# Kernel optimization log

Hardware: AMD Instinct MI355X
Metric: run time of the kernel (lower is better)

The kernel has to match this reference:

```python
import jax, jax.numpy as jnp
import numpy as np

N_NODES = 100000
N_EDGES = 1600000
N_GRAPHS = 512
IN_CH = 128
HID = 128
OUT_CH = 1
FP_DIM = 2048


def prelu(x, a):
    return jnp.where(x > 0, x, a * x)


def setup_inputs() -> dict:
    key = jax.random.key(0)
    ks = jax.random.split(key, 16)

    def glorot(k, shape):
        lim = np.sqrt(6.0 / (shape[0] + shape[1]))
        return jax.random.uniform(k, shape, jnp.float32, -lim, lim)

    x = jax.random.normal(ks[0], (N_NODES, IN_CH), jnp.float32)
    fp = jax.random.normal(ks[1], (N_GRAPHS, FP_DIM), jnp.float32)
    edge_index = jax.random.randint(ks[2], (2, N_EDGES), 0, N_NODES, jnp.int64)
    batch = jnp.sort(jax.random.randint(ks[3], (N_NODES,), 0, N_GRAPHS, jnp.int64))

    params = {
        "W_pre": glorot(ks[4], (IN_CH, HID)),
        "b_pre": jnp.zeros((HID,), jnp.float32),
        "a_pre": jnp.full((HID,), 0.25, jnp.float32),
        "Wl1": glorot(ks[5], (HID, HID)),
        "bl1": jnp.zeros((HID,), jnp.float32),
        "Wr1": glorot(ks[6], (HID, HID)),
        "a1": jnp.full((HID,), 0.25, jnp.float32),
        "Wl2": glorot(ks[7], (HID, HID)),
        "bl2": jnp.zeros((HID,), jnp.float32),
        "Wr2": glorot(ks[8], (HID, HID)),
        "a2": jnp.full((HID,), 0.25, jnp.float32),
        "W_fp": glorot(ks[9], (FP_DIM, HID)),
        "b_fp": jnp.zeros((HID,), jnp.float32),
        "a_fp": jnp.full((HID,), 0.25, jnp.float32),
        "W_post": glorot(ks[10], (2 * HID, OUT_CH)),
        "b_post": jnp.zeros((OUT_CH,), jnp.float32),
    }
    return dict(x=x, fp=fp, edge_index=edge_index, batch=batch, **params)


def sage_conv(x, src, dst, Wl, bl, Wr):
    # aggr='sum': sum messages x[src] into dst, then lin_l(agg)+bias + lin_r(x)
    agg = jax.ops.segment_sum(x[src], dst, num_segments=N_NODES)  # [N, H]
    return agg @ Wl + bl + x @ Wr


def reference(x, fp, edge_index, batch,
              W_pre, b_pre, a_pre,
              Wl1, bl1, Wr1, a1,
              Wl2, bl2, Wr2, a2,
              W_fp, b_fp, a_fp,
              W_post, b_post):
    src, dst = edge_index[0], edge_index[1]
    # pre_mp (dropout is identity at eval)
    h = prelu(x @ W_pre + b_pre, a_pre)
    # message passing
    h = prelu(sage_conv(h, src, dst, Wl1, bl1, Wr1), a1)
    h = prelu(sage_conv(h, src, dst, Wl2, bl2, Wr2), a2)
    # global mean pool over graphs
    sums = jax.ops.segment_sum(h, batch, num_segments=N_GRAPHS)  # [G, H]
    counts = jax.ops.segment_sum(jnp.ones((h.shape[0],), h.dtype), batch,
                                 num_segments=N_GRAPHS)
    pooled = sums / jnp.maximum(counts, 1.0)[:, None]
    # fingerprint head
    fp_emb = prelu(fp @ W_fp + b_fp, a_fp)
    # post mp
    out = jnp.concatenate([pooled, fp_emb], axis=1) @ W_post + b_post
    return out
```

## Files before the change

kernel.cpp:

```cpp
#include <hip/hip_runtime.h>

#define NN 100000
#define NE 1600000
#define NG 512
#define HID 128
#define FPD 2048
#define BSHIFT 8
#define NBUK ((NN + 255) >> 8)
#define BCAP 5120
#define EPB 4096
#define EPT 16

typedef _Float16 f16;
typedef __attribute__((ext_vector_type(8))) _Float16 f16x8;
typedef __attribute__((ext_vector_type(2))) _Float16 f16x2;
typedef __attribute__((ext_vector_type(4))) float f32x4;


__global__ __launch_bounds__(256) void bucket_scatter(const int* __restrict__ src,
                                                      const int* __restrict__ dst,
                                                      int* __restrict__ bcnt,
                                                      uint* __restrict__ bbuf, int E) {
  __shared__ int hist[NBUK];
  __shared__ int gbase[NBUK];
  __shared__ int lbase[NBUK + 1];
  __shared__ int sc[2][512];
  __shared__ uint stage[EPB];
  int t = threadIdx.x;
  int e0 = blockIdx.x * EPB;
  for (int i = t; i < NBUK; i += 256) hist[i] = 0;
  __syncthreads();

  int myb[EPT], myoff[EPT];
  uint myp[EPT];
#pragma unroll
  for (int u = 0; u < EPT; ++u) {
    int e = e0 + u * 256 + t;
    myb[u] = -1;
    if (e < E) {
      int d = dst[e];
      int b = d >> BSHIFT;
      myp[u] = ((uint)(d & 255) << 24) | (uint)src[e];
      myb[u] = b;
      myoff[u] = atomicAdd(&hist[b], 1);
    }
  }
  __syncthreads();

  sc[0][t] = (t < NBUK) ? hist[t] : 0;
  sc[0][t + 256] = (t + 256 < NBUK) ? hist[t + 256] : 0;
  int pp = 0;
  for (int off = 1; off < 512; off <<= 1) {
    __syncthreads();
    int a0 = sc[pp][t] + ((t >= off) ? sc[pp][t - off] : 0);
    int a1 = sc[pp][t + 256] + ((t + 256 >= off) ? sc[pp][t + 256 - off] : 0);
    sc[1 - pp][t] = a0;
    sc[1 - pp][t + 256] = a1;
    pp = 1 - pp;
  }
  __syncthreads();
  if (t < NBUK) lbase[t] = (t == 0) ? 0 : sc[pp][t - 1];
  if (t + 256 < NBUK) lbase[t + 256] = sc[pp][t + 255];
  if (t == 0) lbase[NBUK] = sc[pp][NBUK - 1];
  for (int i = t; i < NBUK; i += 256)
    if (hist[i] > 0) gbase[i] = atomicAdd(&bcnt[i], hist[i]);
  __syncthreads();

#pragma unroll
  for (int u = 0; u < EPT; ++u)
    if (myb[u] >= 0) stage[lbase[myb[u]] + myoff[u]] = myp[u];
  __syncthreads();

  int total = lbase[NBUK];
  for (int j = t; j < total; j += 256) {
    int lo = 0, hi = NBUK - 1;
    while (lo < hi) {
      int mid = (lo + hi + 1) >> 1;
      if (lbase[mid] <= j) lo = mid; else hi = mid - 1;
    }
    bbuf[(size_t)lo * BCAP + gbase[lo] + (j - lbase[lo])] = stage[j];
  }
}

__global__ __launch_bounds__(512) void scan_bcnt(const int* __restrict__ bcnt,
                                                 int* __restrict__ bbase,
                                                 int* __restrict__ rowptr) {
  __shared__ int lds[512];
  int t = threadIdx.x;
  int v = (t < NBUK) ? bcnt[t] : 0;
  lds[t] = v;
  __syncthreads();
  for (int off = 1; off < 512; off <<= 1) {
    int add = (t >= off) ? lds[t - off] : 0;
    __syncthreads();
    lds[t] += add;
    __syncthreads();
  }
  if (t < NBUK) bbase[t] = lds[t] - v;
  if (t == 0) {
    bbase[NBUK] = lds[511];
    rowptr[NN] = lds[511];
  }
}

__global__ __launch_bounds__(256) void bucket_hist_scan(const int* __restrict__ bcnt,
                                                        const uint* __restrict__ bbuf,
                                                        const int* __restrict__ bbase,
                                                        int* __restrict__ rowptr) {
  __shared__ int h[256];
  __shared__ int lds[256];
  int b = blockIdx.x, t = threadIdx.x;
  h[t] = 0;
  __syncthreads();
  int n = bcnt[b];
  const uint* bb = bbuf + (size_t)b * BCAP;
  for (int e = t; e < n; e += 256) atomicAdd(&h[bb[e] >> 24], 1);
  __syncthreads();
  int v = h[t];
  lds[t] = v;
  __syncthreads();
  for (int off = 1; off < 256; off <<= 1) {
    int add = (t >= off) ? lds[t - off] : 0;
    __syncthreads();
    lds[t] += add;
    __syncthreads();
  }
  int node = (b << BSHIFT) + t;
  if (node < NN) rowptr[node] = bbase[b] + lds[t] - v;
}

__global__ __launch_bounds__(256) void bucket_place(const int* __restrict__ bcnt,
                                                    const uint* __restrict__ bbuf,
                                                    const int* __restrict__ rowptr,
                                                    int* __restrict__ cols) {
  __shared__ int cur[256];
  int b = blockIdx.x, t = threadIdx.x;
  int node = (b << BSHIFT) + t;
  cur[t] = rowptr[node < NN ? node : NN];
  __syncthreads();
  int n = bcnt[b];
  const uint* bb = bbuf + (size_t)b * BCAP;
  for (int e = t; e < n; e += 256) {
    uint w = bb[e];
    int pos = atomicAdd(&cur[w >> 24], 1);
    cols[pos] = (int)(w & 0xFFFFFF);
  }
}


__global__ __launch_bounds__(256) void cvt_all(const float* __restrict__ w0,
                                               const float* __restrict__ w1,
                                               const float* __restrict__ w2,
                                               const float* __restrict__ w3,
                                               const float* __restrict__ w4,
                                               const float* __restrict__ Wfp,
                                               const float* __restrict__ fp,
                                               f16* __restrict__ Wt,
                                               f16* __restrict__ Wfpt,
                                               f16* __restrict__ fpb) {
  int idx = blockIdx.x * 256 + threadIdx.x;
  if (idx < 81920) {
    int w = idx >> 14, rem = idx & 16383;
    int j = rem >> 7, k = rem & 127;
    const float* W = (w == 0) ? w0 : (w == 1) ? w1 : (w == 2) ? w2 : (w == 3) ? w3 : w4;
    Wt[idx] = (f16)W[k * 128 + j];
  } else if (idx < 344064) {
    int id = idx - 81920;
    int j = id >> 11, k = id & 2047;
    Wfpt[id] = (f16)Wfp[k * 128 + j];
  } else if (idx < 606208) {
    int id = idx - 344064;
    float4 v = *reinterpret_cast<const float4*>(&fp[id * 4]);
    union { uint2 u; f16 h[4]; } o;
    o.h[0] = (f16)v.x; o.h[1] = (f16)v.y; o.h[2] = (f16)v.z; o.h[3] = (f16)v.w;
    *reinterpret_cast<uint2*>(&fpb[id * 4]) = o.u;
  }
}


__global__ __launch_bounds__(256) void agg_f16(const f16* __restrict__ H,
                                               const int* __restrict__ rowptr,
                                               const int* __restrict__ cols,
                                               f16* __restrict__ out) {
  int node = blockIdx.x * 4 + (threadIdx.x >> 6);
  int lane = threadIdx.x & 63;
  int s = rowptr[node], e = rowptr[node + 1];
  float a0 = 0.f, a1 = 0.f;
  union { uint u; f16x2 h; } cv, cw;
  int i = s;
  for (; i + 7 < e; i += 8) {
    uint uu[8];
#pragma unroll
    for (int q = 0; q < 8; ++q)
      uu[q] = *reinterpret_cast<const uint*>(&H[(size_t)cols[i + q] * 128 + lane * 2]);
    union { uint u; f16x2 h; } t0, t1, t2, t3;
    t0.u = uu[0]; cv.u = uu[1]; t0.h += cv.h;
    t1.u = uu[2]; cv.u = uu[3]; t1.h += cv.h;
    t2.u = uu[4]; cv.u = uu[5]; t2.h += cv.h;
    t3.u = uu[6]; cv.u = uu[7]; t3.h += cv.h;
    a0 += (float)t0.h[0] + (float)t1.h[0] + (float)t2.h[0] + (float)t3.h[0];
    a1 += (float)t0.h[1] + (float)t1.h[1] + (float)t2.h[1] + (float)t3.h[1];
  }
  for (; i + 3 < e; i += 4) {
    uint uu[4];
#pragma unroll
    for (int q = 0; q < 4; ++q)
      uu[q] = *reinterpret_cast<const uint*>(&H[(size_t)cols[i + q] * 128 + lane * 2]);
    union { uint u; f16x2 h; } t0, t1;
    t0.u = uu[0]; cv.u = uu[1]; t0.h += cv.h;
    t1.u = uu[2]; cv.u = uu[3]; t1.h += cv.h;
    a0 += (float)t0.h[0] + (float)t1.h[0];
    a1 += (float)t0.h[1] + (float)t1.h[1];
  }
  for (; i < e; ++i) {
    cw.u = *reinterpret_cast<const uint*>(&H[(size_t)cols[i] * 128 + lane * 2]);
    a0 += (float)cw.h[0]; a1 += (float)cw.h[1];
  }
  union { uint u; f16 h[2]; } pk;
  pk.h[0] = (f16)a0; pk.h[1] = (f16)a1;
  *reinterpret_cast<uint*>(&out[(size_t)node * 128 + lane * 2]) = pk.u;
}


__global__ __launch_bounds__(256) void gemm_pre(const float* __restrict__ X,
                                                const f16* __restrict__ Wt,
                                                const float* __restrict__ bias,
                                                const float* __restrict__ pa,
                                                f16* __restrict__ out, int rows) {
  int t = threadIdx.x;
  int wave = t >> 6, lane = t & 63;
  int lrow = lane & 15, lk = lane >> 4;
  int r0 = blockIdx.x * 128;
  int n0 = wave << 1;

  const f16x8* Wv = reinterpret_cast<const f16x8*>(Wt);
  f16x8 w[2][4];
#pragma unroll
  for (int ni = 0; ni < 2; ++ni)
#pragma unroll
    for (int ks = 0; ks < 4; ++ks)
      w[ni][ks] = Wv[((((n0 + ni) << 4) + lrow) << 4) + (ks << 2) + lk];

  float bv[2], av[2];
#pragma unroll
  for (int ni = 0; ni < 2; ++ni) {
    int col = ((n0 + ni) << 4) + lrow;
    bv[ni] = bias[col];
    av[ni] = pa[col];
  }

#pragma unroll 2
  for (int rg = 0; rg < 8; ++rg) {
    int r = r0 + (rg << 4) + lrow;
    if (r > rows - 1) r = rows - 1;
    const float* xp = X + (size_t)r * 128 + (lk << 3);
    f16x8 a[4];
#pragma unroll
    for (int ks = 0; ks < 4; ++ks) {
      float4 v0 = *reinterpret_cast<const float4*>(xp + (ks << 5));
      float4 v1 = *reinterpret_cast<const float4*>(xp + (ks << 5) + 4);
      f16x8 av8;
      av8[0] = (f16)v0.x; av8[1] = (f16)v0.y; av8[2] = (f16)v0.z; av8[3] = (f16)v0.w;
      av8[4] = (f16)v1.x; av8[5] = (f16)v1.y; av8[6] = (f16)v1.z; av8[7] = (f16)v1.w;
      a[ks] = av8;
    }
    f32x4 acc[2] = {(f32x4){0.f, 0.f, 0.f, 0.f}, (f32x4){0.f, 0.f, 0.f, 0.f}};
#pragma unroll
    for (int ks = 0; ks < 4; ++ks)
#pragma unroll
      for (int ni = 0; ni < 2; ++ni)
        acc[ni] = __builtin_amdgcn_mfma_f32_16x16x32_f16(a[ks], w[ni][ks], acc[ni], 0, 0, 0);
#pragma unroll
    for (int ni = 0; ni < 2; ++ni) {
      int col = ((n0 + ni) << 4) + lrow;
#pragma unroll
      for (int j = 0; j < 4; ++j) {
        int rr = r0 + (rg << 4) + (lk << 2) + j;
        if (rr < rows) {
          float xv = acc[ni][j] + bv[ni];
          xv = xv > 0.f ? xv : av[ni] * xv;
          out[(size_t)rr * 128 + col] = (f16)xv;
        }
      }
    }
  }
}


__global__ __launch_bounds__(256) void gemm_f16(const f16* __restrict__ A1,
                                                const f16* __restrict__ A2,
                                                const f16* __restrict__ W1t,
                                                const f16* __restrict__ W2t,
                                                const float* __restrict__ bias,
                                                const float* __restrict__ pa,
                                                f16* __restrict__ Ch, int rows) {
  int t = threadIdx.x;
  int wave = t >> 6, lane = t & 63;
  int lrow = lane & 15, lk = lane >> 4;
  int r0 = blockIdx.x * 64;
  int n0 = wave << 1;

  const f16x8* Wv1 = reinterpret_cast<const f16x8*>(W1t);
  const f16x8* Wv2 = reinterpret_cast<const f16x8*>(W2t);

  f16x8 w1[2][4], w2[2][4];
#pragma unroll
  for (int ni = 0; ni < 2; ++ni)
#pragma unroll
    for (int ks = 0; ks < 4; ++ks) {
      int wi = ((((n0 + ni) << 4) + lrow) << 4) + (ks << 2) + lk;
      w1[ni][ks] = Wv1[wi];
      w2[ni][ks] = Wv2[wi];
    }

  float bv[2], av[2];
#pragma unroll
  for (int ni = 0; ni < 2; ++ni) {
    int col = ((n0 + ni) << 4) + lrow;
    bv[ni] = bias[col];
    av[ni] = pa[col];
  }

  f16x8 aA[2][4], aB[2][4];
  {
    int r = r0 + lrow;
    if (r > rows - 1) r = rows - 1;
    size_t off = (size_t)r * 128 + (lk << 3);
#pragma unroll
    for (int ks = 0; ks < 4; ++ks) {
      aA[0][ks] = *reinterpret_cast<const f16x8*>(A1 + off + (ks << 5));
      aB[0][ks] = *reinterpret_cast<const f16x8*>(A2 + off + (ks << 5));
    }
  }

#pragma unroll
  for (int rg = 0; rg < 4; ++rg) {
    int cur = rg & 1, nxt = cur ^ 1;
    if (rg < 3) {
      int rn = r0 + ((rg + 1) << 4) + lrow;
      if (rn > rows - 1) rn = rows - 1;
      size_t offn = (size_t)rn * 128 + (lk << 3);
#pragma unroll
      for (int ks = 0; ks < 4; ++ks) {
        aA[nxt][ks] = *reinterpret_cast<const f16x8*>(A1 + offn + (ks << 5));
        aB[nxt][ks] = *reinterpret_cast<const f16x8*>(A2 + offn + (ks << 5));
      }
    }
    f32x4 acc1[2] = {(f32x4){0.f, 0.f, 0.f, 0.f}, (f32x4){0.f, 0.f, 0.f, 0.f}};
    f32x4 acc2[2] = {(f32x4){0.f, 0.f, 0.f, 0.f}, (f32x4){0.f, 0.f, 0.f, 0.f}};
#pragma unroll
    for (int ks = 0; ks < 4; ++ks) {
#pragma unroll
      for (int ni = 0; ni < 2; ++ni) {
        acc1[ni] = __builtin_amdgcn_mfma_f32_16x16x32_f16(aA[cur][ks], w1[ni][ks], acc1[ni], 0, 0, 0);
        acc2[ni] = __builtin_amdgcn_mfma_f32_16x16x32_f16(aB[cur][ks], w2[ni][ks], acc2[ni], 0, 0, 0);
      }
    }
#pragma unroll
    for (int ni = 0; ni < 2; ++ni) {
      int col = ((n0 + ni) << 4) + lrow;
#pragma unroll
      for (int j = 0; j < 4; ++j) {
        int rr = r0 + (rg << 4) + (lk << 2) + j;
        if (rr < rows) {
          float xv = acc1[ni][j] + acc2[ni][j] + bv[ni];
          xv = xv > 0.f ? xv : av[ni] * xv;
          Ch[(size_t)rr * 128 + col] = (f16)xv;
        }
      }
    }
  }
}


__global__ __launch_bounds__(256) void fp_gemm(const f16* __restrict__ A,
                                               const f16* __restrict__ Wt,
                                               float* __restrict__ part) {
  int kc = blockIdx.x;
  int rb = blockIdx.y;
  int t = threadIdx.x;
  int wave = t >> 6, lane = t & 63;
  int lrow = lane & 15, lk = lane >> 4;
  int r0 = rb * 128;
  int n0 = wave << 1;

  const f16x8* Wv = reinterpret_cast<const f16x8*>(Wt);
  const f16x8* Av = reinterpret_cast<const f16x8*>(A);

  f16x8 w[2][4];
#pragma unroll
  for (int ni = 0; ni < 2; ++ni)
#pragma unroll
    for (int ks = 0; ks < 4; ++ks) {
      int j = ((n0 + ni) << 4) + lrow;
      w[ni][ks] = Wv[j * 256 + (kc << 4) + (ks << 2) + lk];
    }

#pragma unroll 2
  for (int rg = 0; rg < 8; ++rg) {
    int r = r0 + (rg << 4) + lrow;
    f16x8 a[4];
#pragma unroll
    for (int ks = 0; ks < 4; ++ks)
      a[ks] = Av[r * 256 + (kc << 4) + (ks << 2) + lk];
    f32x4 acc[2] = {(f32x4){0.f, 0.f, 0.f, 0.f}, (f32x4){0.f, 0.f, 0.f, 0.f}};
#pragma unroll
    for (int ks = 0; ks < 4; ++ks)
#pragma unroll
      for (int ni = 0; ni < 2; ++ni)
        acc[ni] = __builtin_amdgcn_mfma_f32_16x16x32_f16(a[ks], w[ni][ks], acc[ni], 0, 0, 0);
#pragma unroll
    for (int ni = 0; ni < 2; ++ni) {
      int col = ((n0 + ni) << 4) + lrow;
#pragma unroll
      for (int j = 0; j < 4; ++j) {
        int rr = r0 + (rg << 4) + (lk << 2) + j;
        part[((size_t)kc * 512 + rr) * 128 + col] = acc[ni][j];
      }
    }
  }
}


__device__ __forceinline__ int lower_bound_dev(const int* __restrict__ arr, int n, int val) {
  int lo = 0, hi = n;
  while (lo < hi) {
    int mid = (lo + hi) >> 1;
    if (arr[mid] < val) lo = mid + 1; else hi = mid;
  }
  return lo;
}

__global__ __launch_bounds__(512) void pool_final(const f16* __restrict__ H,
                                                  const int* __restrict__ batch,
                                                  const float* __restrict__ part,
                                                  const float* __restrict__ bfp,
                                                  const float* __restrict__ afp,
                                                  const float* __restrict__ Wp,
                                                  const float* __restrict__ bp,
                                                  float* __restrict__ out) {
  __shared__ float red[512];
  __shared__ float pf[256];
  int g = blockIdx.x;
  int t = threadIdx.x;
  int col = t & 127, rq = t >> 7;
  int start = lower_bound_dev(batch, NN, g);
  int end = lower_bound_dev(batch, NN, g + 1);
  float acc = 0.f;
  for (int r = start + rq; r < end; r += 4) acc += (float)H[(size_t)r * 128 + col];
  red[t] = acc;
  __syncthreads();
  if (t < 128) {
    float s = red[t] + red[128 + t] + red[256 + t] + red[384 + t];
    int c = end - start;
    pf[t] = s / (float)(c > 0 ? c : 1);
  } else if (t < 256) {
    int j = t - 128;
    float s = bfp[j];
#pragma unroll
    for (int kc = 0; kc < 16; ++kc) s += part[((size_t)kc * 512 + g) * 128 + j];
    float a = afp[j];
    pf[t] = s > 0.f ? s : a * s;
  }
  __syncthreads();
  if (t < 128) {
    float v = pf[t] * Wp[t] + pf[128 + t] * Wp[128 + t];
    red[t] = v;
  }
  __syncthreads();
  if (t < 64) {
    float v = red[t] + red[t + 64];
    for (int off = 32; off > 0; off >>= 1) v += __shfl_down(v, off);
    if (t == 0) out[g] = v + bp[0];
  }
}


extern "C" void kernel_launch(void* const* d_in, const int* in_sizes, int n_in,
                              void* d_out, int out_size, void* d_ws, size_t ws_size,
                              hipStream_t stream) {
  const float* x      = (const float*)d_in[0];
  const float* fp     = (const float*)d_in[1];
  const int*   ei     = (const int*)d_in[2];
  const int*   batch  = (const int*)d_in[3];
  const float* W_pre  = (const float*)d_in[4];
  const float* b_pre  = (const float*)d_in[5];
  const float* a_pre  = (const float*)d_in[6];
  const float* Wl1    = (const float*)d_in[7];
  const float* bl1    = (const float*)d_in[8];
  const float* Wr1    = (const float*)d_in[9];
  const float* a1     = (const float*)d_in[10];
  const float* Wl2    = (const float*)d_in[11];
  const float* bl2    = (const float*)d_in[12];
  const float* Wr2    = (const float*)d_in[13];
  const float* a2     = (const float*)d_in[14];
  const float* W_fp   = (const float*)d_in[15];
  const float* b_fp   = (const float*)d_in[16];
  const float* a_fp   = (const float*)d_in[17];
  const float* W_post = (const float*)d_in[18];
  const float* b_post = (const float*)d_in[19];

  const int* src = ei;
  const int* dst = ei + NE;

  const size_t NBUF = (size_t)NN * 128;
  f16* bufA = (f16*)d_ws;
  f16* bufB = bufA + NBUF;
  f16* bufC = bufB + NBUF;
  f16* Wt   = bufC + NBUF;
  f16* fpb  = Wt + 5 * 16384;
  f16* Wfpt = fpb + 512 * 2048;
  float* part = (float*)(Wfpt + 128 * 2048);
  int* rowptr  = (int*)(part + 16 * 512 * 128);
  int* bbase   = rowptr + NN + 4;
  int* bcnt    = bbase + NBUK + 4;
  int* colsA   = bcnt + ((NBUK + 3) & ~3);
  uint* bbuf   = (uint*)(colsA + NE);

  hipMemsetAsync(bcnt, 0, NBUK * sizeof(int), stream);
  bucket_scatter<<<(NE + EPB - 1) / EPB, 256, 0, stream>>>(src, dst, bcnt, bbuf, NE);
  scan_bcnt<<<1, 512, 0, stream>>>(bcnt, bbase, rowptr);
  bucket_hist_scan<<<NBUK, 256, 0, stream>>>(bcnt, bbuf, bbase, rowptr);
  bucket_place<<<NBUK, 256, 0, stream>>>(bcnt, bbuf, rowptr, colsA);

  cvt_all<<<(606208 + 255) / 256, 256, 0, stream>>>(W_pre, Wl1, Wr1, Wl2, Wr2, W_fp, fp,
                                                    Wt, Wfpt, fpb);
  {
    dim3 g(16, 4);
    fp_gemm<<<g, 256, 0, stream>>>(fpb, Wfpt, part);
  }

  const f16* Wt_pre = Wt;
  const f16* Wt_l1  = Wt + 16384;
  const f16* Wt_r1  = Wt + 32768;
  const f16* Wt_l2  = Wt + 49152;
  const f16* Wt_r2  = Wt + 65536;

  gemm_pre<<<(NN + 127) / 128, 256, 0, stream>>>(x, Wt_pre, b_pre, a_pre, bufA, NN);

  int gGemm = (NN + 63) / 64;

  agg_f16<<<NN / 4, 256, 0, stream>>>(bufA, rowptr, colsA, bufC);
  gemm_f16<<<gGemm, 256, 0, stream>>>(bufC, bufA, Wt_l1, Wt_r1, bl1, a1, bufB, NN);

  agg_f16<<<NN / 4, 256, 0, stream>>>(bufB, rowptr, colsA, bufC);
  gemm_f16<<<gGemm, 256, 0, stream>>>(bufC, bufB, Wt_l2, Wt_r2, bl2, a2, bufA, NN);

  pool_final<<<NG, 512, 0, stream>>>(bufA, batch, part, b_fp, a_fp, W_post, b_post,
                                     (float*)d_out);
}
```

Baseline: 336.7 us.

## Fuse bucket histogram and placement kernels; widen aggregation gathers to 16-byte loads

The separate histogram/scan and placement kernels are merged into one kernel that caches each bucket's edges in LDS, so the bucket buffer is read from global memory once and one launch is dropped. The aggregation kernel now has each quarter-wave handle a different neighbor with 16-byte loads of eight halves per lane, then reduces the partial sums across quarter-waves with shuffles. This cuts the number of gather instructions per edge and the per-row index loads. The cost is 8 float accumulators per lane, the cross-lane reduction, and an idle-lane tail for degrees that are not multiples of four.

```diff
diff --git a/kernel.cpp b/kernel.cpp
--- a/kernel.cpp
+++ b/kernel.cpp
@@ -13,7 +13,6 @@
 
 typedef _Float16 f16;
 typedef __attribute__((ext_vector_type(8))) _Float16 f16x8;
-typedef __attribute__((ext_vector_type(2))) _Float16 f16x2;
 typedef __attribute__((ext_vector_type(4))) float f32x4;
 
 
@@ -103,45 +102,42 @@
   }
 }
 
-__global__ __launch_bounds__(256) void bucket_hist_scan(const int* __restrict__ bcnt,
-                                                        const uint* __restrict__ bbuf,
-                                                        const int* __restrict__ bbase,
-                                                        int* __restrict__ rowptr) {
+__global__ __launch_bounds__(256) void bucket_finish(const int* __restrict__ bcnt,
+                                                     const uint* __restrict__ bbuf,
+                                                     const int* __restrict__ bbase,
+                                                     int* __restrict__ rowptr,
+                                                     int* __restrict__ cols) {
+  __shared__ uint ebuf[BCAP];
   __shared__ int h[256];
-  __shared__ int lds[256];
+  __shared__ int s2[256];
+  __shared__ int cur[256];
   int b = blockIdx.x, t = threadIdx.x;
   h[t] = 0;
-  __syncthreads();
-  int n = bcnt[b];
-  const uint* bb = bbuf + (size_t)b * BCAP;
-  for (int e = t; e < n; e += 256) atomicAdd(&h[bb[e] >> 24], 1);
-  __syncthreads();
-  int v = h[t];
-  lds[t] = v;
-  __syncthreads();
-  for (int off = 1; off < 256; off <<= 1) {
-    int add = (t >= off) ? lds[t - off] : 0;
-    __syncthreads();
-    lds[t] += add;
-    __syncthreads();
-  }
-  int node = (b << BSHIFT) + t;
-  if (node < NN) rowptr[node] = bbase[b] + lds[t] - v;
-}
-
-__global__ __launch_bounds__(256) void bucket_place(const int* __restrict__ bcnt,
-                                                    const uint* __restrict__ bbuf,
-                                                    const int* __restrict__ rowptr,
-                                                    int* __restrict__ cols) {
-  __shared__ int cur[256];
-  int b = blockIdx.x, t = threadIdx.x;
-  int node = (b << BSHIFT) + t;
-  cur[t] = rowptr[node < NN ? node : NN];
   __syncthreads();
   int n = bcnt[b];
   const uint* bb = bbuf + (size_t)b * BCAP;
   for (int e = t; e < n; e += 256) {
     uint w = bb[e];
+    ebuf[e] = w;
+    atomicAdd(&h[w >> 24], 1);
+  }
+  __syncthreads();
+  int v = h[t];
+  s2[t] = v;
+  __syncthreads();
+  for (int off = 1; off < 256; off <<= 1) {
+    int add = (t >= off) ? s2[t - off] : 0;
+    __syncthreads();
+    s2[t] += add;
+    __syncthreads();
+  }
+  int base = bbase[b] + s2[t] - v;
+  int node = (b << BSHIFT) + t;
+  if (node < NN) rowptr[node] = base;
+  cur[t] = base;
+  __syncthreads();
+  for (int e = t; e < n; e += 256) {
+    uint w = ebuf[e];
     int pos = atomicAdd(&cur[w >> 24], 1);
     cols[pos] = (int)(w & 0xFFFFFF);
   }
@@ -184,41 +180,46 @@
                                                f16* __restrict__ out) {
   int node = blockIdx.x * 4 + (threadIdx.x >> 6);
   int lane = threadIdx.x & 63;
+  int q = lane >> 4;
+  int sub = lane & 15;
   int s = rowptr[node], e = rowptr[node + 1];
-  float a0 = 0.f, a1 = 0.f;
-  union { uint u; f16x2 h; } cv, cw;
+  float acc[8] = {0.f, 0.f, 0.f, 0.f, 0.f, 0.f, 0.f, 0.f};
+  union { uint4 u; f16 h[8]; } cv;
+
   int i = s;
   for (; i + 7 < e; i += 8) {
-    uint uu[8];
-#pragma unroll
-    for (int q = 0; q < 8; ++q)
-      uu[q] = *reinterpret_cast<const uint*>(&H[(size_t)cols[i + q] * 128 + lane * 2]);
-    union { uint u; f16x2 h; } t0, t1, t2, t3;
-    t0.u = uu[0]; cv.u = uu[1]; t0.h += cv.h;
-    t1.u = uu[2]; cv.u = uu[3]; t1.h += cv.h;
-    t2.u = uu[4]; cv.u = uu[5]; t2.h += cv.h;
-    t3.u = uu[6]; cv.u = uu[7]; t3.h += cv.h;
-    a0 += (float)t0.h[0] + (float)t1.h[0] + (float)t2.h[0] + (float)t3.h[0];
-    a1 += (float)t0.h[1] + (float)t1.h[1] + (float)t2.h[1] + (float)t3.h[1];
-  }
-  for (; i + 3 < e; i += 4) {
-    uint uu[4];
-#pragma unroll
-    for (int q = 0; q < 4; ++q)
-      uu[q] = *reinterpret_cast<const uint*>(&H[(size_t)cols[i + q] * 128 + lane * 2]);
-    union { uint u; f16x2 h; } t0, t1;
-    t0.u = uu[0]; cv.u = uu[1]; t0.h += cv.h;
-    t1.u = uu[2]; cv.u = uu[3]; t1.h += cv.h;
-    a0 += (float)t0.h[0] + (float)t1.h[0];
-    a1 += (float)t0.h[1] + (float)t1.h[1];
-  }
-  for (; i < e; ++i) {
-    cw.u = *reinterpret_cast<const uint*>(&H[(size_t)cols[i] * 128 + lane * 2]);
-    a0 += (float)cw.h[0]; a1 += (float)cw.h[1];
-  }
-  union { uint u; f16 h[2]; } pk;
-  pk.h[0] = (f16)a0; pk.h[1] = (f16)a1;
-  *reinterpret_cast<uint*>(&out[(size_t)node * 128 + lane * 2]) = pk.u;
+    int c0 = cols[i + q];
+    int c1 = cols[i + 4 + q];
+    uint4 v0 = *reinterpret_cast<const uint4*>(&H[(size_t)c0 * 128 + sub * 8]);
+    uint4 v1 = *reinterpret_cast<const uint4*>(&H[(size_t)c1 * 128 + sub * 8]);
+    cv.u = v0;
+#pragma unroll
+    for (int z = 0; z < 8; ++z) acc[z] += (float)cv.h[z];
+    cv.u = v1;
+#pragma unroll
+    for (int z = 0; z < 8; ++z) acc[z] += (float)cv.h[z];
+  }
+  for (; i < e; i += 4) {
+    int rem = e - i;
+    if (q < rem) {
+      int c = cols[i + q];
+      cv.u = *reinterpret_cast<const uint4*>(&H[(size_t)c * 128 + sub * 8]);
+#pragma unroll
+      for (int z = 0; z < 8; ++z) acc[z] += (float)cv.h[z];
+    }
+  }
+
+#pragma unroll
+  for (int z = 0; z < 8; ++z) {
+    acc[z] += __shfl_xor(acc[z], 16);
+    acc[z] += __shfl_xor(acc[z], 32);
+  }
+  if (q == 0) {
+    union { uint4 u; f16 h[8]; } pk;
+#pragma unroll
+    for (int z = 0; z < 8; ++z) pk.h[z] = (f16)acc[z];
+    *reinterpret_cast<uint4*>(&out[(size_t)node * 128 + sub * 8]) = pk.u;
+  }
 }
 
 
@@ -520,8 +521,7 @@
   hipMemsetAsync(bcnt, 0, NBUK * sizeof(int), stream);
   bucket_scatter<<<(NE + EPB - 1) / EPB, 256, 0, stream>>>(src, dst, bcnt, bbuf, NE);
   scan_bcnt<<<1, 512, 0, stream>>>(bcnt, bbase, rowptr);
-  bucket_hist_scan<<<NBUK, 256, 0, stream>>>(bcnt, bbuf, bbase, rowptr);
-  bucket_place<<<NBUK, 256, 0, stream>>>(bcnt, bbuf, rowptr, colsA);
+  bucket_finish<<<NBUK, 256, 0, stream>>>(bcnt, bbuf, bbase, rowptr, colsA);
 
   cvt_all<<<(606208 + 255) / 256, 256, 0, stream>>>(W_pre, Wl1, Wr1, Wl2, Wr2, W_fp, fp,
                                                     Wt, Wfpt, fpb);
```

Result: no change. 330.9 us (-1.7%).
